# Kernel optimization log

Measured on AMD Instinct MI355X. Metric: run time of the kernel, lower is better.

## Reference

```python
import jax, jax.numpy as jnp
import numpy as np

N_POINTS = 262144
L_LEVELS = 16
FEATS_PER_LEVEL = 2
BASE_RES = 8
FINEST_RES = 512
TABLE_SIZE = 2 ** 12  # log2_hashmap_size = 12
HIDDEN = 256
IN_FEATURES = 3
MLP_IN = L_LEVELS * FEATS_PER_LEVEL + IN_FEATURES - 2  # 33


def _level_params():
    b = np.exp((np.log(FINEST_RES) - np.log(BASE_RES)) / (L_LEVELS - 1))
    res = np.floor(BASE_RES * b ** np.arange(L_LEVELS)).astype(np.int64)
    hsize = np.minimum(res ** 2, TABLE_SIZE)  # per-level hashmap size
    return jnp.asarray(res, jnp.float32), jnp.asarray(hsize, jnp.uint32)


RES, HSIZE = _level_params()
PRIMES = jnp.array([1, 2654435761], dtype=jnp.uint32)  # instant-NGP spatial hash primes (2D)
CORNERS = jnp.array([[0, 0], [0, 1], [1, 0], [1, 1]], dtype=jnp.int32)  # [4,2]


def hash_encode(coords, tables):
    # coords: [N,2] in [0,1]; tables: [L, TABLE_SIZE, F]
    x = coords[None, :, :] * RES[:, None, None]            # [L,N,2] scaled per level
    xi = jnp.floor(x)
    xf = x - xi                                            # fractional part (grad flows to coords)
    inds = xi.astype(jnp.int32)[:, :, None, :] + CORNERS   # [L,N,4,2] corner integer coords
    # bilinear weights: offset 0 -> (1-xf), offset 1 -> xf
    w = jnp.prod(jnp.where(CORNERS == 0, 1.0 - xf[:, :, None, :], xf[:, :, None, :]), axis=-1)  # [L,N,4]
    u = inds.astype(jnp.uint32) * PRIMES                   # [L,N,4,2]
    h = (u[..., 0] ^ u[..., 1]) % HSIZE[:, None, None]     # [L,N,4] hashed table index
    feats = jax.vmap(lambda t, i: t[i])(tables, h)         # [L,N,4,F] gather per level
    out = jnp.einsum('lncf,lnc->lnf', feats, w)            # [L,N,F] bilinear interp
    return jnp.moveaxis(out, 0, 1).reshape(coords.shape[0], -1)  # [N, L*F], level-major per point


def reference(x, tables, W0, b0, W1, b1, W2, b2, W3, b3, W4, b4):
    h = hash_encode(x[:, :2], tables)                      # [N, 32]
    h = jnp.concatenate([h, x[:, 2:]], axis=-1)            # [N, 33]
    h = jax.nn.relu(h @ W0 + b0)
    h = jax.nn.relu(h @ W1 + b1)
    h = jax.nn.relu(h @ W2 + b2)
    h = jax.nn.relu(h @ W3 + b3)
    return h @ W4 + b4                                     # [N, 1]


def setup_inputs() -> dict:
    key = jax.random.key(0)
    ks = jax.random.split(key, 12)

    def lin(kw, fan_in, fan_out):
        s = 1.0 / np.sqrt(fan_in)
        return jax.random.normal(kw, (fan_in, fan_out), jnp.float32) * s

    return {
        'x': jax.random.uniform(ks[0], (N_POINTS, IN_FEATURES), jnp.float32),
        'tables': jax.random.normal(ks[1], (L_LEVELS, TABLE_SIZE, FEATS_PER_LEVEL), jnp.float32) * 1e-2,
        'W0': lin(ks[2], MLP_IN, HIDDEN), 'b0': jnp.zeros((HIDDEN,), jnp.float32),
        'W1': lin(ks[3], HIDDEN, HIDDEN), 'b1': jnp.zeros((HIDDEN,), jnp.float32),
        'W2': lin(ks[4], HIDDEN, HIDDEN), 'b2': jnp.zeros((HIDDEN,), jnp.float32),
        'W3': lin(ks[5], HIDDEN, HIDDEN), 'b3': jnp.zeros((HIDDEN,), jnp.float32),
        'W4': lin(ks[6], HIDDEN, 1),      'b4': jnp.zeros((1,), jnp.float32),
    }
```

## Files before the change

kernel.cpp:

```cpp
#include <hip/hip_runtime.h>
#include <math.h>


typedef __bf16 bf16x8 __attribute__((ext_vector_type(8)));
typedef float  f32x16 __attribute__((ext_vector_type(16)));
typedef unsigned int u32x4 __attribute__((ext_vector_type(4)));
typedef unsigned int u32x2 __attribute__((ext_vector_type(2)));

struct LevelParams {
  float res[16];
  unsigned hsize[16];
  unsigned M[8];
  unsigned c16[8];
  int      sh[8];
};

static constexpr int MTILE = 64;
static constexpr int LDA   = 264;
static constexpr int ACT_ELEMS = MTILE * LDA;
static constexpr int UB_L0 = 0, UB_L1 = 24, UB_L2 = 152, UB_L3 = 280;
static constexpr int UNITS_TOTAL = 408;

__device__ __forceinline__ unsigned short f32_to_bf16_rne(float f) {
  unsigned u = __float_as_uint(f);
  unsigned r = (u + 0x7fffu + ((u >> 16) & 1u)) >> 16;
  return (unsigned short)r;
}
__device__ __forceinline__ float bf16_bits_to_f32(unsigned u16bits) {
  return __uint_as_float(u16bits << 16);
}
__device__ __forceinline__ unsigned pack_hi(unsigned u0, unsigned u1) {
  return (u0 >> 16) | (u1 & 0xffff0000u);
}

__global__ void prep_pack(const float* __restrict__ W0, const float* __restrict__ W1,
                          const float* __restrict__ W2, const float* __restrict__ W3,
                          unsigned short* __restrict__ pack) {
  int b = blockIdx.x;
  int l = threadIdx.x;
  const float* W; int K, s, cq;
  if (b < UB_L1) { W = W0; K = 33; s = b >> 3; cq = b & 7; }
  else {
    int b2 = b - UB_L1; int ly = b2 >> 7; int r = b2 & 127;
    W = (ly == 0) ? W1 : (ly == 1) ? W2 : W3; K = 256; s = r >> 3; cq = r & 7;
  }
  int col = (cq << 5) + (l & 31);
  int kb  = (s << 4) + ((l >> 5) << 3);
  unsigned short* dst = pack + (size_t)b * 1024 + l * 8;
#pragma unroll
  for (int e = 0; e < 8; ++e) {
    int k = kb + e;
    float v = (k < K) ? W[k * 256 + col] : 0.0f;
    unsigned u = __float_as_uint(v);
    unsigned short h = (unsigned short)(u >> 16);
    float hf = bf16_bits_to_f32(u >> 16);
    unsigned short lo = f32_to_bf16_rne(v - hf);
    dst[e]       = h;
    dst[512 + e] = lo;
  }
}

template<int S>
__device__ __forceinline__ void run_layer(unsigned short* __restrict__ ahi,
                                          unsigned short* __restrict__ alo,
                                          const unsigned short* __restrict__ pack,
                                          int ubase,
                                          const float* __restrict__ bias,
                                          int cq, int l) {
  f32x16 acc0 = (f32x16)0.0f, acc1 = (f32x16)0.0f;
  const int i31 = l & 31, p = l >> 5;

  const unsigned short* a0h = ahi + i31 * LDA + (p << 3);
  const unsigned short* a1h = ahi + (32 + i31) * LDA + (p << 3);
  const unsigned short* a0l = alo + i31 * LDA + (p << 3);
  const unsigned short* a1l = alo + (32 + i31) * LDA + (p << 3);
  const unsigned short* wb  = pack + (size_t)(ubase + cq) * 1024 + l * 8;

  u32x4 wh = *(const u32x4*)(wb);
  u32x4 wl = *(const u32x4*)(wb + 512);
#pragma unroll
  for (int s = 0; s < S; ++s) {
    u32x4 whn = wh, wln = wl;
    if (s + 1 < S) {
      whn = *(const u32x4*)(wb + (size_t)(s + 1) * 8192);
      wln = *(const u32x4*)(wb + (size_t)(s + 1) * 8192 + 512);
    }
    bf16x8 ah0 = __builtin_bit_cast(bf16x8, *(const u32x4*)(a0h + (s << 4)));
    bf16x8 al0 = __builtin_bit_cast(bf16x8, *(const u32x4*)(a0l + (s << 4)));
    bf16x8 ah1 = __builtin_bit_cast(bf16x8, *(const u32x4*)(a1h + (s << 4)));
    bf16x8 al1 = __builtin_bit_cast(bf16x8, *(const u32x4*)(a1l + (s << 4)));
    bf16x8 W_h = __builtin_bit_cast(bf16x8, wh);
    bf16x8 W_l = __builtin_bit_cast(bf16x8, wl);
    acc0 = __builtin_amdgcn_mfma_f32_32x32x16_bf16(W_h, ah0, acc0, 0, 0, 0);
    acc1 = __builtin_amdgcn_mfma_f32_32x32x16_bf16(W_h, ah1, acc1, 0, 0, 0);
    acc0 = __builtin_amdgcn_mfma_f32_32x32x16_bf16(W_l, ah0, acc0, 0, 0, 0);
    acc1 = __builtin_amdgcn_mfma_f32_32x32x16_bf16(W_l, ah1, acc1, 0, 0, 0);
    acc0 = __builtin_amdgcn_mfma_f32_32x32x16_bf16(W_h, al0, acc0, 0, 0, 0);
    acc1 = __builtin_amdgcn_mfma_f32_32x32x16_bf16(W_h, al1, acc1, 0, 0, 0);
    wh = whn; wl = wln;
  }
  __syncthreads();

#pragma unroll
  for (int pt = 0; pt < 2; ++pt) {
    int arow = (pt << 5) + i31;
    f32x16 A = pt ? acc1 : acc0;
#pragma unroll
    for (int g = 0; g < 4; ++g) {
      int chb = (cq << 5) + (g << 3) + (p << 2);
      float4 bv = *(const float4*)(bias + chb);
      float v0 = fmaxf(A[4 * g + 0] + bv.x, 0.0f);
      float v1 = fmaxf(A[4 * g + 1] + bv.y, 0.0f);
      float v2 = fmaxf(A[4 * g + 2] + bv.z, 0.0f);
      float v3 = fmaxf(A[4 * g + 3] + bv.w, 0.0f);
      unsigned u0 = __float_as_uint(v0), u1 = __float_as_uint(v1);
      unsigned u2 = __float_as_uint(v2), u3 = __float_as_uint(v3);
      u32x2 hw = { pack_hi(u0, u1), pack_hi(u2, u3) };
      float l0 = v0 - __uint_as_float(u0 & 0xffff0000u);
      float l1 = v1 - __uint_as_float(u1 & 0xffff0000u);
      float l2 = v2 - __uint_as_float(u2 & 0xffff0000u);
      float l3 = v3 - __uint_as_float(u3 & 0xffff0000u);
      u32x2 lw = { pack_hi(__float_as_uint(l0), __float_as_uint(l1)),
                   pack_hi(__float_as_uint(l2), __float_as_uint(l3)) };
      int base = arow * LDA + chb;
      *(u32x2*)(ahi + base) = hw;
      *(u32x2*)(alo + base) = lw;
    }
  }
  __syncthreads();
}

__global__ __launch_bounds__(512, 4) void inr_main(
    const float* __restrict__ x, const float* __restrict__ tables,
    const float* __restrict__ b0, const float* __restrict__ b1,
    const float* __restrict__ b2, const float* __restrict__ b3,
    const float* __restrict__ W4, const float* __restrict__ b4,
    const unsigned short* __restrict__ pack, float* __restrict__ out,
    LevelParams P) {
  extern __shared__ char smem[];
  unsigned short* ahi = (unsigned short*)smem;
  unsigned short* alo = ahi + ACT_ELEMS;

  const int tid = threadIdx.x;

  {
    int pl = tid >> 3, q = tid & 7;
    size_t pidx = (size_t)blockIdx.x * MTILE + pl;
    float x0 = x[3 * pidx + 0], x1 = x[3 * pidx + 1], x2 = x[3 * pidx + 2];
    float f_lo0, f_lo1, f_hi0, f_hi1;

    {
      float rf = P.res[q];
      unsigned d = P.hsize[q], c = P.c16[q], M = P.M[q];
      int sh = P.sh[q];
      float xs0 = x0 * rf, xs1 = x1 * rf;
      float fl0 = floorf(xs0), fl1 = floorf(xs1);
      float f0 = xs0 - fl0, f1 = xs1 - fl1;
      int i0 = (int)fl0, i1 = (int)fl1;
      unsigned ua0 = (unsigned)i0, ua1 = (unsigned)(i0 + 1);
      unsigned vb0 = (unsigned)i1 * 2654435761u;
      unsigned vb1 = (unsigned)(i1 + 1) * 2654435761u;
      const float* tl = tables + ((size_t)q << 13);
      float g0 = 1.0f - f0, g1 = 1.0f - f1;
      unsigned e0 = ua0 ^ vb0, e1 = ua0 ^ vb1, e2 = ua1 ^ vb0, e3 = ua1 ^ vb1;
      unsigned n0 = (e0 >> 16) * c + (e0 & 0xffffu);
      unsigned n1 = (e1 >> 16) * c + (e1 & 0xffffu);
      unsigned n2 = (e2 >> 16) * c + (e2 & 0xffffu);
      unsigned n3 = (e3 >> 16) * c + (e3 & 0xffffu);
      unsigned h0 = n0 - (__umulhi(n0, M) >> sh) * d;
      unsigned h1 = n1 - (__umulhi(n1, M) >> sh) * d;
      unsigned h2 = n2 - (__umulhi(n2, M) >> sh) * d;
      unsigned h3 = n3 - (__umulhi(n3, M) >> sh) * d;
      float a0 = 0.0f, a1 = 0.0f;
      { float w = g0 * g1; a0 += w * tl[2*h0]; a1 += w * tl[2*h0+1]; }
      { float w = g0 * f1; a0 += w * tl[2*h1]; a1 += w * tl[2*h1+1]; }
      { float w = f0 * g1; a0 += w * tl[2*h2]; a1 += w * tl[2*h2+1]; }
      { float w = f0 * f1; a0 += w * tl[2*h3]; a1 += w * tl[2*h3+1]; }
      f_lo0 = a0; f_lo1 = a1;
    }
    {
      int lv = q + 8;
      float rf = P.res[lv];
      float xs0 = x0 * rf, xs1 = x1 * rf;
      float fl0 = floorf(xs0), fl1 = floorf(xs1);
      float f0 = xs0 - fl0, f1 = xs1 - fl1;
      int i0 = (int)fl0, i1 = (int)fl1;
      unsigned ua0 = (unsigned)i0, ua1 = (unsigned)(i0 + 1);
      unsigned vb0 = (unsigned)i1 * 2654435761u;
      unsigned vb1 = (unsigned)(i1 + 1) * 2654435761u;
      const float* tl = tables + ((size_t)lv << 13);
      float g0 = 1.0f - f0, g1 = 1.0f - f1;
      unsigned h0 = (ua0 ^ vb0) & 4095u, h1 = (ua0 ^ vb1) & 4095u;
      unsigned h2 = (ua1 ^ vb0) & 4095u, h3 = (ua1 ^ vb1) & 4095u;
      float a0 = 0.0f, a1 = 0.0f;
      { float w = g0 * g1; a0 += w * tl[2*h0]; a1 += w * tl[2*h0+1]; }
      { float w = g0 * f1; a0 += w * tl[2*h1]; a1 += w * tl[2*h1+1]; }
      { float w = f0 * g1; a0 += w * tl[2*h2]; a1 += w * tl[2*h2+1]; }
      { float w = f0 * f1; a0 += w * tl[2*h3]; a1 += w * tl[2*h3+1]; }
      f_hi0 = a0; f_hi1 = a1;
    }
    {
      int rowb = pl * LDA;
      unsigned u0 = __float_as_uint(f_lo0), u1 = __float_as_uint(f_lo1);
      unsigned u2 = __float_as_uint(f_hi0), u3 = __float_as_uint(f_hi1);
      float l0 = f_lo0 - __uint_as_float(u0 & 0xffff0000u);
      float l1 = f_lo1 - __uint_as_float(u1 & 0xffff0000u);
      float l2 = f_hi0 - __uint_as_float(u2 & 0xffff0000u);
      float l3 = f_hi1 - __uint_as_float(u3 & 0xffff0000u);
      *(unsigned*)(ahi + rowb + 2*q)      = pack_hi(u0, u1);
      *(unsigned*)(ahi + rowb + 16 + 2*q) = pack_hi(u2, u3);
      *(unsigned*)(alo + rowb + 2*q)      = pack_hi(__float_as_uint(l0), __float_as_uint(l1));
      *(unsigned*)(alo + rowb + 16 + 2*q) = pack_hi(__float_as_uint(l2), __float_as_uint(l3));
    }
    {
      int base = pl * LDA + 32 + 2*q;
      if (q == 0) {
        unsigned u0 = __float_as_uint(x2);
        float l0 = x2 - __uint_as_float(u0 & 0xffff0000u);
        *(unsigned*)(ahi + base) = u0 >> 16;
        *(unsigned*)(alo + base) = __float_as_uint(l0) >> 16;
      } else {
        *(unsigned*)(ahi + base) = 0u;
        *(unsigned*)(alo + base) = 0u;
      }
    }
  }
  __syncthreads();

  const int l  = tid & 63;
  const int cq = tid >> 6;

  run_layer<3>(ahi, alo, pack, UB_L0, b0, cq, l);
  run_layer<16>(ahi, alo, pack, UB_L1, b1, cq, l);
  run_layer<16>(ahi, alo, pack, UB_L2, b2, cq, l);
  run_layer<16>(ahi, alo, pack, UB_L3, b3, cq, l);

  {
    int pl = tid >> 3, q = tid & 7;
    const unsigned short* hrow = ahi + pl * LDA + (q << 5);
    const unsigned short* lrow = alo + pl * LDA + (q << 5);
    const float* w4p = W4 + (q << 5);
    float sum = 0.0f;
#pragma unroll
    for (int c = 0; c < 4; ++c) {
      u32x4 th = *(const u32x4*)(hrow + (c << 3));
      u32x4 tl = *(const u32x4*)(lrow + (c << 3));
      float4 wA = *(const float4*)(w4p + (c << 3));
      float4 wB = *(const float4*)(w4p + (c << 3) + 4);
#pragma unroll
      for (int u = 0; u < 4; ++u) {
        unsigned hu = th[u], lu = tl[u];
        float v0 = __uint_as_float(hu << 16) + __uint_as_float(lu << 16);
        float v1 = __uint_as_float(hu & 0xffff0000u) + __uint_as_float(lu & 0xffff0000u);
        const float* wp = (u < 2) ? &wA.x : &wB.x;
        int base = (u & 1) << 1;
        sum = fmaf(v0, wp[base], sum);
        sum = fmaf(v1, wp[base + 1], sum);
      }
    }
    sum += __shfl_xor(sum, 1);
    sum += __shfl_xor(sum, 2);
    sum += __shfl_xor(sum, 4);
    if (q == 0) out[(size_t)blockIdx.x * MTILE + pl] = sum + b4[0];
  }
}

extern "C" void kernel_launch(void* const* d_in, const int* in_sizes, int n_in,
                              void* d_out, int out_size, void* d_ws, size_t ws_size,
                              hipStream_t stream) {
  const float* x      = (const float*)d_in[0];
  const float* tables = (const float*)d_in[1];
  const float* W0 = (const float*)d_in[2];  const float* b0 = (const float*)d_in[3];
  const float* W1 = (const float*)d_in[4];  const float* b1 = (const float*)d_in[5];
  const float* W2 = (const float*)d_in[6];  const float* b2 = (const float*)d_in[7];
  const float* W3 = (const float*)d_in[8];  const float* b3 = (const float*)d_in[9];
  const float* W4 = (const float*)d_in[10]; const float* b4 = (const float*)d_in[11];
  unsigned short* pack = (unsigned short*)d_ws;
  float* out = (float*)d_out;

  LevelParams P;
  double bgrow = exp((log(512.0) - log(8.0)) / 15.0);
  for (int lvl = 0; lvl < 16; ++lvl) {
    double r = floor(8.0 * pow(bgrow, (double)lvl));
    P.res[lvl] = (float)r;
    double hsd = r * r;
    if (hsd > 4096.0) hsd = 4096.0;
    P.hsize[lvl] = (unsigned)hsd;
  }
  for (int lvl = 0; lvl < 8; ++lvl) {
    unsigned d = P.hsize[lvl];
    P.c16[lvl] = 65536u % d;
    unsigned long long nmax = 65535ULL * d;
    int s = 0;
    while (nmax * d >= (1ULL << (32 + s))) s++;
    P.sh[lvl] = s;
    P.M[lvl] = (unsigned)((1ULL << (32 + s)) / d + 1);
  }

  prep_pack<<<UNITS_TOTAL, 64, 0, stream>>>(W0, W1, W2, W3, pack);

  size_t smem_bytes = (size_t)ACT_ELEMS * 2 * 2;
  hipFuncSetAttribute(reinterpret_cast<const void*>(inr_main),
                      hipFuncAttributeMaxDynamicSharedMemorySize, (int)smem_bytes);

  int nblocks = out_size / MTILE;
  inr_main<<<nblocks, 512, smem_bytes, stream>>>(x, tables, b0, b1, b2, b3, W4, b4,
                                                 pack, out, P);
}
```

Before: 308.9 us.

## Halve block size and give each wave a 64x64 tile with triple-buffered operands

Each block now runs 4 waves (256 threads) instead of 8, and each wave computes two 32-column groups for both 32-row halves. The A fragments loaded from LDS are reused across twice as many output columns. Weight and activation loads are prefetched two k-steps ahead through a three-slot register ring. The encoding and final reduction stages are remapped to 4 threads per point. This cuts LDS reads per MFMA and hides load latency, at the cost of many more registers (4 accumulators plus the prefetch buffers) and fewer waves per block to hide latency.

Result: faster. 296.4 us (-4.0%).

```diff
diff --git a/kernel.cpp b/kernel.cpp
--- a/kernel.cpp
+++ b/kernel.cpp
@@ -60,77 +60,166 @@
   }
 }
 
+__device__ __forceinline__ void enc_magic(float x0, float x1, const LevelParams& P,
+                                          int lvl, const float* __restrict__ tables,
+                                          float& o0, float& o1) {
+  float rf = P.res[lvl];
+  unsigned d = P.hsize[lvl], c = P.c16[lvl], M = P.M[lvl];
+  int sh = P.sh[lvl];
+  float xs0 = x0 * rf, xs1 = x1 * rf;
+  float fl0 = floorf(xs0), fl1 = floorf(xs1);
+  float f0 = xs0 - fl0, f1 = xs1 - fl1;
+  int i0 = (int)fl0, i1 = (int)fl1;
+  unsigned ua0 = (unsigned)i0, ua1 = (unsigned)(i0 + 1);
+  unsigned vb0 = (unsigned)i1 * 2654435761u;
+  unsigned vb1 = (unsigned)(i1 + 1) * 2654435761u;
+  const float* tl = tables + ((size_t)lvl << 13);
+  float g0 = 1.0f - f0, g1 = 1.0f - f1;
+  unsigned e0 = ua0 ^ vb0, e1 = ua0 ^ vb1, e2 = ua1 ^ vb0, e3 = ua1 ^ vb1;
+  unsigned n0 = (e0 >> 16) * c + (e0 & 0xffffu);
+  unsigned n1 = (e1 >> 16) * c + (e1 & 0xffffu);
+  unsigned n2 = (e2 >> 16) * c + (e2 & 0xffffu);
+  unsigned n3 = (e3 >> 16) * c + (e3 & 0xffffu);
+  unsigned h0 = n0 - (__umulhi(n0, M) >> sh) * d;
+  unsigned h1 = n1 - (__umulhi(n1, M) >> sh) * d;
+  unsigned h2 = n2 - (__umulhi(n2, M) >> sh) * d;
+  unsigned h3 = n3 - (__umulhi(n3, M) >> sh) * d;
+  float a0 = 0.0f, a1 = 0.0f;
+  { float w = g0 * g1; a0 += w * tl[2*h0]; a1 += w * tl[2*h0+1]; }
+  { float w = g0 * f1; a0 += w * tl[2*h1]; a1 += w * tl[2*h1+1]; }
+  { float w = f0 * g1; a0 += w * tl[2*h2]; a1 += w * tl[2*h2+1]; }
+  { float w = f0 * f1; a0 += w * tl[2*h3]; a1 += w * tl[2*h3+1]; }
+  o0 = a0; o1 = a1;
+}
+__device__ __forceinline__ void enc_and(float x0, float x1, const LevelParams& P,
+                                        int lvl, const float* __restrict__ tables,
+                                        float& o0, float& o1) {
+  float rf = P.res[lvl];
+  float xs0 = x0 * rf, xs1 = x1 * rf;
+  float fl0 = floorf(xs0), fl1 = floorf(xs1);
+  float f0 = xs0 - fl0, f1 = xs1 - fl1;
+  int i0 = (int)fl0, i1 = (int)fl1;
+  unsigned ua0 = (unsigned)i0, ua1 = (unsigned)(i0 + 1);
+  unsigned vb0 = (unsigned)i1 * 2654435761u;
+  unsigned vb1 = (unsigned)(i1 + 1) * 2654435761u;
+  const float* tl = tables + ((size_t)lvl << 13);
+  float g0 = 1.0f - f0, g1 = 1.0f - f1;
+  unsigned h0 = (ua0 ^ vb0) & 4095u, h1 = (ua0 ^ vb1) & 4095u;
+  unsigned h2 = (ua1 ^ vb0) & 4095u, h3 = (ua1 ^ vb1) & 4095u;
+  float a0 = 0.0f, a1 = 0.0f;
+  { float w = g0 * g1; a0 += w * tl[2*h0]; a1 += w * tl[2*h0+1]; }
+  { float w = g0 * f1; a0 += w * tl[2*h1]; a1 += w * tl[2*h1+1]; }
+  { float w = f0 * g1; a0 += w * tl[2*h2]; a1 += w * tl[2*h2+1]; }
+  { float w = f0 * f1; a0 += w * tl[2*h3]; a1 += w * tl[2*h3+1]; }
+  o0 = a0; o1 = a1;
+}
+__device__ __forceinline__ void store_pair(unsigned short* ahi, unsigned short* alo,
+                                           int idx, float v0, float v1) {
+  unsigned u0 = __float_as_uint(v0), u1 = __float_as_uint(v1);
+  float l0 = v0 - __uint_as_float(u0 & 0xffff0000u);
+  float l1 = v1 - __uint_as_float(u1 & 0xffff0000u);
+  *(unsigned*)(ahi + idx) = pack_hi(u0, u1);
+  *(unsigned*)(alo + idx) = pack_hi(__float_as_uint(l0), __float_as_uint(l1));
+}
+
 template<int S>
 __device__ __forceinline__ void run_layer(unsigned short* __restrict__ ahi,
                                           unsigned short* __restrict__ alo,
                                           const unsigned short* __restrict__ pack,
                                           int ubase,
                                           const float* __restrict__ bias,
-                                          int cq, int l) {
-  f32x16 acc0 = (f32x16)0.0f, acc1 = (f32x16)0.0f;
+                                          int cg, int l) {
+  f32x16 acc00 = (f32x16)0.0f, acc01 = (f32x16)0.0f;
+  f32x16 acc10 = (f32x16)0.0f, acc11 = (f32x16)0.0f;
   const int i31 = l & 31, p = l >> 5;
 
   const unsigned short* a0h = ahi + i31 * LDA + (p << 3);
   const unsigned short* a1h = ahi + (32 + i31) * LDA + (p << 3);
   const unsigned short* a0l = alo + i31 * LDA + (p << 3);
   const unsigned short* a1l = alo + (32 + i31) * LDA + (p << 3);
-  const unsigned short* wb  = pack + (size_t)(ubase + cq) * 1024 + l * 8;
-
-  u32x4 wh = *(const u32x4*)(wb);
-  u32x4 wl = *(const u32x4*)(wb + 512);
+  const unsigned short* wb  = pack + (size_t)(ubase + (cg << 1)) * 1024 + l * 8;
+
+  u32x4 A[3][4];
+  u32x4 W[3][4];
+
+#define LOADSTEP(j, st)                                                        \
+  do {                                                                         \
+    A[j][0] = *(const u32x4*)(a0h + ((st) << 4));                              \
+    A[j][1] = *(const u32x4*)(a0l + ((st) << 4));                              \
+    A[j][2] = *(const u32x4*)(a1h + ((st) << 4));                              \
+    A[j][3] = *(const u32x4*)(a1l + ((st) << 4));                              \
+    const unsigned short* wp = wb + (size_t)(st) * 8192;                       \
+    W[j][0] = *(const u32x4*)(wp);                                             \
+    W[j][1] = *(const u32x4*)(wp + 512);                                       \
+    W[j][2] = *(const u32x4*)(wp + 1024);                                      \
+    W[j][3] = *(const u32x4*)(wp + 1536);                                      \
+  } while (0)
+
+  LOADSTEP(0, 0);
+  if (S > 1) LOADSTEP(1, 1);
+
 #pragma unroll
   for (int s = 0; s < S; ++s) {
-    u32x4 whn = wh, wln = wl;
-    if (s + 1 < S) {
-      whn = *(const u32x4*)(wb + (size_t)(s + 1) * 8192);
-      wln = *(const u32x4*)(wb + (size_t)(s + 1) * 8192 + 512);
+    if (s + 2 < S) { const int j = (s + 2) % 3; LOADSTEP(j, s + 2); }
+    const int sl = s % 3;
+    bf16x8 AH0 = __builtin_bit_cast(bf16x8, A[sl][0]);
+    bf16x8 AL0 = __builtin_bit_cast(bf16x8, A[sl][1]);
+    bf16x8 AH1 = __builtin_bit_cast(bf16x8, A[sl][2]);
+    bf16x8 AL1 = __builtin_bit_cast(bf16x8, A[sl][3]);
+    bf16x8 Wh0 = __builtin_bit_cast(bf16x8, W[sl][0]);
+    bf16x8 Wl0 = __builtin_bit_cast(bf16x8, W[sl][1]);
+    bf16x8 Wh1 = __builtin_bit_cast(bf16x8, W[sl][2]);
+    bf16x8 Wl1 = __builtin_bit_cast(bf16x8, W[sl][3]);
+    acc00 = __builtin_amdgcn_mfma_f32_32x32x16_bf16(Wh0, AH0, acc00, 0, 0, 0);
+    acc01 = __builtin_amdgcn_mfma_f32_32x32x16_bf16(Wh1, AH0, acc01, 0, 0, 0);
+    acc10 = __builtin_amdgcn_mfma_f32_32x32x16_bf16(Wh0, AH1, acc10, 0, 0, 0);
+    acc11 = __builtin_amdgcn_mfma_f32_32x32x16_bf16(Wh1, AH1, acc11, 0, 0, 0);
+    acc00 = __builtin_amdgcn_mfma_f32_32x32x16_bf16(Wl0, AH0, acc00, 0, 0, 0);
+    acc01 = __builtin_amdgcn_mfma_f32_32x32x16_bf16(Wl1, AH0, acc01, 0, 0, 0);
+    acc10 = __builtin_amdgcn_mfma_f32_32x32x16_bf16(Wl0, AH1, acc10, 0, 0, 0);
+    acc11 = __builtin_amdgcn_mfma_f32_32x32x16_bf16(Wl1, AH1, acc11, 0, 0, 0);
+    acc00 = __builtin_amdgcn_mfma_f32_32x32x16_bf16(Wh0, AL0, acc00, 0, 0, 0);
+    acc01 = __builtin_amdgcn_mfma_f32_32x32x16_bf16(Wh1, AL0, acc01, 0, 0, 0);
+    acc10 = __builtin_amdgcn_mfma_f32_32x32x16_bf16(Wh0, AL1, acc10, 0, 0, 0);
+    acc11 = __builtin_amdgcn_mfma_f32_32x32x16_bf16(Wh1, AL1, acc11, 0, 0, 0);
+  }
+#undef LOADSTEP
+  __syncthreads();
+
+#pragma unroll
+  for (int pt = 0; pt < 2; ++pt) {
+#pragma unroll
+    for (int c = 0; c < 2; ++c) {
+      f32x16 Acc = pt ? (c ? acc11 : acc10) : (c ? acc01 : acc00);
+      int arow = (pt << 5) + i31;
+      int colb = (cg << 6) + (c << 5) + (p << 2);
+#pragma unroll
+      for (int g = 0; g < 4; ++g) {
+        int chb = colb + (g << 3);
+        float4 bv = *(const float4*)(bias + chb);
+        float v0 = fmaxf(Acc[4 * g + 0] + bv.x, 0.0f);
+        float v1 = fmaxf(Acc[4 * g + 1] + bv.y, 0.0f);
+        float v2 = fmaxf(Acc[4 * g + 2] + bv.z, 0.0f);
+        float v3 = fmaxf(Acc[4 * g + 3] + bv.w, 0.0f);
+        unsigned u0 = __float_as_uint(v0), u1 = __float_as_uint(v1);
+        unsigned u2 = __float_as_uint(v2), u3 = __float_as_uint(v3);
+        u32x2 hw = { pack_hi(u0, u1), pack_hi(u2, u3) };
+        float l0 = v0 - __uint_as_float(u0 & 0xffff0000u);
+        float l1 = v1 - __uint_as_float(u1 & 0xffff0000u);
+        float l2 = v2 - __uint_as_float(u2 & 0xffff0000u);
+        float l3 = v3 - __uint_as_float(u3 & 0xffff0000u);
+        u32x2 lw = { pack_hi(__float_as_uint(l0), __float_as_uint(l1)),
+                     pack_hi(__float_as_uint(l2), __float_as_uint(l3)) };
+        int base = arow * LDA + chb;
+        *(u32x2*)(ahi + base) = hw;
+        *(u32x2*)(alo + base) = lw;
+      }
     }
-    bf16x8 ah0 = __builtin_bit_cast(bf16x8, *(const u32x4*)(a0h + (s << 4)));
-    bf16x8 al0 = __builtin_bit_cast(bf16x8, *(const u32x4*)(a0l + (s << 4)));
-    bf16x8 ah1 = __builtin_bit_cast(bf16x8, *(const u32x4*)(a1h + (s << 4)));
-    bf16x8 al1 = __builtin_bit_cast(bf16x8, *(const u32x4*)(a1l + (s << 4)));
-    bf16x8 W_h = __builtin_bit_cast(bf16x8, wh);
-    bf16x8 W_l = __builtin_bit_cast(bf16x8, wl);
-    acc0 = __builtin_amdgcn_mfma_f32_32x32x16_bf16(W_h, ah0, acc0, 0, 0, 0);
-    acc1 = __builtin_amdgcn_mfma_f32_32x32x16_bf16(W_h, ah1, acc1, 0, 0, 0);
-    acc0 = __builtin_amdgcn_mfma_f32_32x32x16_bf16(W_l, ah0, acc0, 0, 0, 0);
-    acc1 = __builtin_amdgcn_mfma_f32_32x32x16_bf16(W_l, ah1, acc1, 0, 0, 0);
-    acc0 = __builtin_amdgcn_mfma_f32_32x32x16_bf16(W_h, al0, acc0, 0, 0, 0);
-    acc1 = __builtin_amdgcn_mfma_f32_32x32x16_bf16(W_h, al1, acc1, 0, 0, 0);
-    wh = whn; wl = wln;
   }
   __syncthreads();
-
-#pragma unroll
-  for (int pt = 0; pt < 2; ++pt) {
-    int arow = (pt << 5) + i31;
-    f32x16 A = pt ? acc1 : acc0;
-#pragma unroll
-    for (int g = 0; g < 4; ++g) {
-      int chb = (cq << 5) + (g << 3) + (p << 2);
-      float4 bv = *(const float4*)(bias + chb);
-      float v0 = fmaxf(A[4 * g + 0] + bv.x, 0.0f);
-      float v1 = fmaxf(A[4 * g + 1] + bv.y, 0.0f);
-      float v2 = fmaxf(A[4 * g + 2] + bv.z, 0.0f);
-      float v3 = fmaxf(A[4 * g + 3] + bv.w, 0.0f);
-      unsigned u0 = __float_as_uint(v0), u1 = __float_as_uint(v1);
-      unsigned u2 = __float_as_uint(v2), u3 = __float_as_uint(v3);
-      u32x2 hw = { pack_hi(u0, u1), pack_hi(u2, u3) };
-      float l0 = v0 - __uint_as_float(u0 & 0xffff0000u);
-      float l1 = v1 - __uint_as_float(u1 & 0xffff0000u);
-      float l2 = v2 - __uint_as_float(u2 & 0xffff0000u);
-      float l3 = v3 - __uint_as_float(u3 & 0xffff0000u);
-      u32x2 lw = { pack_hi(__float_as_uint(l0), __float_as_uint(l1)),
-                   pack_hi(__float_as_uint(l2), __float_as_uint(l3)) };
-      int base = arow * LDA + chb;
-      *(u32x2*)(ahi + base) = hw;
-      *(u32x2*)(alo + base) = lw;
-    }
-  }
-  __syncthreads();
-}
-
-__global__ __launch_bounds__(512, 4) void inr_main(
+}
+
+__global__ __launch_bounds__(256, 2) void inr_main(
     const float* __restrict__ x, const float* __restrict__ tables,
     const float* __restrict__ b0, const float* __restrict__ b1,
     const float* __restrict__ b2, const float* __restrict__ b3,
@@ -144,105 +233,47 @@
   const int tid = threadIdx.x;
 
   {
-    int pl = tid >> 3, q = tid & 7;
+    int pl = tid >> 2, q = tid & 3;
     size_t pidx = (size_t)blockIdx.x * MTILE + pl;
     float x0 = x[3 * pidx + 0], x1 = x[3 * pidx + 1], x2 = x[3 * pidx + 2];
-    float f_lo0, f_lo1, f_hi0, f_hi1;
-
-    {
-      float rf = P.res[q];
-      unsigned d = P.hsize[q], c = P.c16[q], M = P.M[q];
-      int sh = P.sh[q];
-      float xs0 = x0 * rf, xs1 = x1 * rf;
-      float fl0 = floorf(xs0), fl1 = floorf(xs1);
-      float f0 = xs0 - fl0, f1 = xs1 - fl1;
-      int i0 = (int)fl0, i1 = (int)fl1;
-      unsigned ua0 = (unsigned)i0, ua1 = (unsigned)(i0 + 1);
-      unsigned vb0 = (unsigned)i1 * 2654435761u;
-      unsigned vb1 = (unsigned)(i1 + 1) * 2654435761u;
-      const float* tl = tables + ((size_t)q << 13);
-      float g0 = 1.0f - f0, g1 = 1.0f - f1;
-      unsigned e0 = ua0 ^ vb0, e1 = ua0 ^ vb1, e2 = ua1 ^ vb0, e3 = ua1 ^ vb1;
-      unsigned n0 = (e0 >> 16) * c + (e0 & 0xffffu);
-      unsigned n1 = (e1 >> 16) * c + (e1 & 0xffffu);
-      unsigned n2 = (e2 >> 16) * c + (e2 & 0xffffu);
-      unsigned n3 = (e3 >> 16) * c + (e3 & 0xffffu);
-      unsigned h0 = n0 - (__umulhi(n0, M) >> sh) * d;
-      unsigned h1 = n1 - (__umulhi(n1, M) >> sh) * d;
-      unsigned h2 = n2 - (__umulhi(n2, M) >> sh) * d;
-      unsigned h3 = n3 - (__umulhi(n3, M) >> sh) * d;
-      float a0 = 0.0f, a1 = 0.0f;
-      { float w = g0 * g1; a0 += w * tl[2*h0]; a1 += w * tl[2*h0+1]; }
-      { float w = g0 * f1; a0 += w * tl[2*h1]; a1 += w * tl[2*h1+1]; }
-      { float w = f0 * g1; a0 += w * tl[2*h2]; a1 += w * tl[2*h2+1]; }
-      { float w = f0 * f1; a0 += w * tl[2*h3]; a1 += w * tl[2*h3+1]; }
-      f_lo0 = a0; f_lo1 = a1;
+    int rowb = pl * LDA;
+    float o0, o1;
+    enc_magic(x0, x1, P, q,      tables, o0, o1); store_pair(ahi, alo, rowb + 2*q,      o0, o1);
+    enc_magic(x0, x1, P, q + 4,  tables, o0, o1); store_pair(ahi, alo, rowb + 8 + 2*q,  o0, o1);
+    enc_and  (x0, x1, P, q + 8,  tables, o0, o1); store_pair(ahi, alo, rowb + 16 + 2*q, o0, o1);
+    enc_and  (x0, x1, P, q + 12, tables, o0, o1); store_pair(ahi, alo, rowb + 24 + 2*q, o0, o1);
+    int base = rowb + 32 + (q << 2);
+    if (q == 0) {
+      unsigned u0 = __float_as_uint(x2);
+      float l0 = x2 - __uint_as_float(u0 & 0xffff0000u);
+      u32x2 hw = { u0 >> 16, 0u };
+      u32x2 lw = { __float_as_uint(l0) >> 16, 0u };
+      *(u32x2*)(ahi + base) = hw;
+      *(u32x2*)(alo + base) = lw;
+    } else {
+      u32x2 z = { 0u, 0u };
+      *(u32x2*)(ahi + base) = z;
+      *(u32x2*)(alo + base) = z;
     }
-    {
-      int lv = q + 8;
-      float rf = P.res[lv];
-      float xs0 = x0 * rf, xs1 = x1 * rf;
-      float fl0 = floorf(xs0), fl1 = floorf(xs1);
-      float f0 = xs0 - fl0, f1 = xs1 - fl1;
-      int i0 = (int)fl0, i1 = (int)fl1;
-      unsigned ua0 = (unsigned)i0, ua1 = (unsigned)(i0 + 1);
-      unsigned vb0 = (unsigned)i1 * 2654435761u;
-      unsigned vb1 = (unsigned)(i1 + 1) * 2654435761u;
-      const float* tl = tables + ((size_t)lv << 13);
-      float g0 = 1.0f - f0, g1 = 1.0f - f1;
-      unsigned h0 = (ua0 ^ vb0) & 4095u, h1 = (ua0 ^ vb1) & 4095u;
-      unsigned h2 = (ua1 ^ vb0) & 4095u, h3 = (ua1 ^ vb1) & 4095u;
-      float a0 = 0.0f, a1 = 0.0f;
-      { float w = g0 * g1; a0 += w * tl[2*h0]; a1 += w * tl[2*h0+1]; }
-      { float w = g0 * f1; a0 += w * tl[2*h1]; a1 += w * tl[2*h1+1]; }
-      { float w = f0 * g1; a0 += w * tl[2*h2]; a1 += w * tl[2*h2+1]; }
-      { float w = f0 * f1; a0 += w * tl[2*h3]; a1 += w * tl[2*h3+1]; }
-      f_hi0 = a0; f_hi1 = a1;
-    }
-    {
-      int rowb = pl * LDA;
-      unsigned u0 = __float_as_uint(f_lo0), u1 = __float_as_uint(f_lo1);
-      unsigned u2 = __float_as_uint(f_hi0), u3 = __float_as_uint(f_hi1);
-      float l0 = f_lo0 - __uint_as_float(u0 & 0xffff0000u);
-      float l1 = f_lo1 - __uint_as_float(u1 & 0xffff0000u);
-      float l2 = f_hi0 - __uint_as_float(u2 & 0xffff0000u);
-      float l3 = f_hi1 - __uint_as_float(u3 & 0xffff0000u);
-      *(unsigned*)(ahi + rowb + 2*q)      = pack_hi(u0, u1);
-      *(unsigned*)(ahi + rowb + 16 + 2*q) = pack_hi(u2, u3);
-      *(unsigned*)(alo + rowb + 2*q)      = pack_hi(__float_as_uint(l0), __float_as_uint(l1));
-      *(unsigned*)(alo + rowb + 16 + 2*q) = pack_hi(__float_as_uint(l2), __float_as_uint(l3));
-    }
-    {
-      int base = pl * LDA + 32 + 2*q;
-      if (q == 0) {
-        unsigned u0 = __float_as_uint(x2);
-        float l0 = x2 - __uint_as_float(u0 & 0xffff0000u);
-        *(unsigned*)(ahi + base) = u0 >> 16;
-        *(unsigned*)(alo + base) = __float_as_uint(l0) >> 16;
-      } else {
-        *(unsigned*)(ahi + base) = 0u;
-        *(unsigned*)(alo + base) = 0u;
-      }
-    }
   }
   __syncthreads();
 
   const int l  = tid & 63;
-  const int cq = tid >> 6;
-
-  run_layer<3>(ahi, alo, pack, UB_L0, b0, cq, l);
-  run_layer<16>(ahi, alo, pack, UB_L1, b1, cq, l);
-  run_layer<16>(ahi, alo, pack, UB_L2, b2, cq, l);
-  run_layer<16>(ahi, alo, pack, UB_L3, b3, cq, l);
+  const int cg = tid >> 6;
+
+  run_layer<3>(ahi, alo, pack, UB_L0, b0, cg, l);
+  run_layer<16>(ahi, alo, pack, UB_L1, b1, cg, l);
+  run_layer<16>(ahi, alo, pack, UB_L2, b2, cg, l);
+  run_layer<16>(ahi, alo, pack, UB_L3, b3, cg, l);
 
   {
-    int pl = tid >> 3, q = tid & 7;
-    const unsigned short* hrow = ahi + pl * LDA + (q << 5);
-    const unsigned short* lrow = alo + pl * LDA + (q << 5);
-    const float* w4p = W4 + (q << 5);
+    int pl = tid >> 2, q = tid & 3;
+    const unsigned short* hrow = ahi + pl * LDA + (q << 6);
+    const unsigned short* lrow = alo + pl * LDA + (q << 6);
+    const float* w4p = W4 + (q << 6);
     float sum = 0.0f;
 #pragma unroll
-    for (int c = 0; c < 4; ++c) {
+    for (int c = 0; c < 8; ++c) {
       u32x4 th = *(const u32x4*)(hrow + (c << 3));
       u32x4 tl = *(const u32x4*)(lrow + (c << 3));
       float4 wA = *(const float4*)(w4p + (c << 3));
@@ -260,7 +291,6 @@
     }
     sum += __shfl_xor(sum, 1);
     sum += __shfl_xor(sum, 2);
-    sum += __shfl_xor(sum, 4);
     if (q == 0) out[(size_t)blockIdx.x * MTILE + pl] = sum + b4[0];
   }
 }
@@ -304,6 +334,6 @@
                       hipFuncAttributeMaxDynamicSharedMemorySize, (int)smem_bytes);
 
   int nblocks = out_size / MTILE;
-  inr_main<<<nblocks, 512, smem_bytes, stream>>>(x, tables, b0, b1, b2, b3, W4, b4,
+  inr_main<<<nblocks, 256, smem_bytes, stream>>>(x, tables, b0, b1, b2, b3, W4, b4,
                                                  pack, out, P);
 }
```
